# Kernel tuning notes

Measured on AMD Instinct MI355X. Metric: run time of the kernel, lower is better.

## Reference

```python
import jax, jax.numpy as jnp
import numpy as np

STATE_DIM = 1024
INPUT_DIM = 1024
OUTPUT_DIM = 1024
BATCH = 8
SEQ = 2048


def setup_inputs() -> dict:
    key = jax.random.key(0)
    k_x, k_a, k_b, k_w, k_bias = jax.random.split(key, 5)
    x = jax.random.normal(k_x, (BATCH, SEQ, INPUT_DIM), dtype=jnp.float32)
    # diagonal transition a in (0, 0.99) for stability
    A = jax.random.uniform(k_a, (STATE_DIM,), dtype=jnp.float32, minval=0.0, maxval=0.99)
    B = jax.random.normal(k_b, (STATE_DIM, INPUT_DIM), dtype=jnp.float32) / np.sqrt(INPUT_DIM)
    W = jax.random.normal(k_w, (OUTPUT_DIM, STATE_DIM), dtype=jnp.float32) / np.sqrt(STATE_DIM)
    b = jax.random.normal(k_bias, (OUTPUT_DIM,), dtype=jnp.float32) * 0.01
    return {"x": x, "A": A, "B": B, "W": W, "b": b}


def reference(x, A, B, W, b):
    # x: [batch, seq, input_dim]
    # Input projection: u_t = B x_t  -> [batch, seq, state_dim]
    u = jnp.einsum('bld,nd->bln', x, B)
    # Diagonal linear recurrence h_t = A * h_{t-1} + u_t via associative scan.
    # Pair representation (a, b) composes as (a1*a2, a2*b1 + b2).
    aa = jnp.broadcast_to(A, u.shape)

    def combine(c1, c2):
        a1, b1 = c1
        a2, b2 = c2
        return a1 * a2, a2 * b1 + b2

    _, h = jax.lax.associative_scan(combine, (aa, u), axis=1)
    # Output projection: [batch, seq, output_dim]
    return jnp.einsum('bln,on->blo', h, W) + b
```

## Files before the change

kernel.cpp:

```cpp
#include <hip/hip_runtime.h>
#include <stdint.h>

#define BATCH 8
#define SEQ 2048
#define DIM 1024
#define MTOT (BATCH * SEQ)

typedef __attribute__((ext_vector_type(8))) short short8;
typedef __attribute__((ext_vector_type(8))) unsigned short ushort8;
typedef __attribute__((ext_vector_type(4))) float floatx4;


__device__ __forceinline__ unsigned short f2bf(float f) {
  union { float f; unsigned u; } c; c.f = f;
  unsigned u = c.u;
  return (unsigned short)((u + 0x7FFFu + ((u >> 16) & 1u)) >> 16);
}
__device__ __forceinline__ float bf2f(unsigned short h) {
  union { unsigned u; float f; } c; c.u = ((unsigned)h) << 16;
  return c.f;
}

__device__ __forceinline__ void gll16(const void* g, void* l) {
  __builtin_amdgcn_global_load_lds(
      (__attribute__((address_space(1))) void*)(uintptr_t)g,
      (__attribute__((address_space(3))) void*)(uintptr_t)l,
      16, 0, 0);
}


#define X4 (MTOT * DIM / 4)
#define M4 (DIM * DIM / 4)

__global__ __launch_bounds__(256) void cast3_kernel(
    const float* __restrict__ x, const float* __restrict__ B,
    const float* __restrict__ W, unsigned short* __restrict__ xb,
    unsigned short* __restrict__ Bb, unsigned short* __restrict__ Wb) {
  int i = blockIdx.x * 256 + threadIdx.x;
  const float4* s4;
  uint2* d2;
  int li;
  if (i < X4) {
    s4 = (const float4*)x; d2 = (uint2*)xb; li = i;
  } else if (i < X4 + M4) {
    s4 = (const float4*)B; d2 = (uint2*)Bb; li = i - X4;
  } else {
    s4 = (const float4*)W; d2 = (uint2*)Wb; li = i - X4 - M4;
  }
  float4 v = s4[li];
  uint2 o;
  o.x = (unsigned)f2bf(v.x) | ((unsigned)f2bf(v.y) << 16);
  o.y = (unsigned)f2bf(v.z) | ((unsigned)f2bf(v.w) << 16);
  d2[li] = o;
}


__global__ __launch_bounds__(256) void gemm1_fused(
    const unsigned short* __restrict__ A,
    const unsigned short* __restrict__ B,
    unsigned short* __restrict__ u,
    const float* __restrict__ Adiag,
    float* __restrict__ aggbuf) {
  __shared__ unsigned short smem[16384];
  __shared__ float segsum[2][128];
  unsigned short* sA = smem;
  unsigned short* sB = smem + 8192;

  const int tid = threadIdx.x;
  const int wave = tid >> 6, lane = tid & 63;

  const int id = blockIdx.x;
  const int xcd = id & 7, j = id >> 3;
  const int mt = xcd * 16 + (j >> 3);
  const int nt = j & 7;
  const size_t m0 = (size_t)mt * 128;
  const int n0 = nt * 128;

  floatx4 acc[4][4] = {};

  const int srow = wave * 8 + (lane >> 3);
  const int scol = (((lane & 7) ^ ((lane >> 3) & 7)) * 8);
  const unsigned short* gA = A + (m0 + srow) * 1024 + scol;
  const unsigned short* gB = B + ((size_t)n0 + srow) * 1024 + scol;
  unsigned short* lA = sA + wave * 8 * 64;
  unsigned short* lB = sB + wave * 8 * 64;

  const int fr = lane & 15;
  const int frs = fr & 7;
  const int kb = lane >> 4;
  const int wm = (wave & 1) * 64, wn = (wave >> 1) * 64;

  for (int kt = 0; kt < 1024; kt += 64) {
#pragma unroll
    for (int r = 0; r < 4; ++r) {
      gll16(gA + (size_t)r * 32 * 1024 + kt, lA + r * 32 * 64);
      gll16(gB + (size_t)r * 32 * 1024 + kt, lB + r * 32 * 64);
    }
    asm volatile("s_waitcnt vmcnt(0)" ::: "memory");
    __syncthreads();
#pragma unroll
    for (int kk = 0; kk < 64; kk += 32) {
      short8 af[4], bfv[4];
#pragma unroll
      for (int i = 0; i < 4; ++i)
        af[i] = *(const short8*)(sA + (wm + i * 16 + fr) * 64 +
                                 ((((kk >> 3) + kb) ^ frs) * 8));
#pragma unroll
      for (int jj = 0; jj < 4; ++jj)
        bfv[jj] = *(const short8*)(sB + (wn + jj * 16 + fr) * 64 +
                                   ((((kk >> 3) + kb) ^ frs) * 8));
#pragma unroll
      for (int i = 0; i < 4; ++i)
#pragma unroll
        for (int jj = 0; jj < 4; ++jj)
          acc[i][jj] = __builtin_amdgcn_mfma_f32_16x16x32_bf16(
              af[i], bfv[jj], acc[i][jj], 0, 0, 0);
    }
    __syncthreads();
  }

  const int col = lane & 15;
  const int row4 = (lane >> 4) * 4;
  unsigned short* sC = smem;
#pragma unroll
  for (int i = 0; i < 4; ++i)
#pragma unroll
    for (int jj = 0; jj < 4; ++jj)
#pragma unroll
      for (int r = 0; r < 4; ++r)
        sC[(wm + i * 16 + row4 + r) * 128 + wn + jj * 16 + col] =
            f2bf(acc[i][jj][r]);
  __syncthreads();

  const int colv = tid & 127;
  const int seg = tid >> 7;
  const float a = Adiag[n0 + colv];
  {
    float s = 0.f;
    const int t0 = seg * 64;
#pragma unroll 8
    for (int t = 0; t < 64; ++t) {
      int idx = (t0 + t) * 128 + colv;
      s = fmaf(a, s, bf2f(sC[idx]));
      sC[idx] = f2bf(s);
    }
    segsum[seg][colv] = s;
  }
  __syncthreads();

  {
    float a2 = a * a, a4 = a2 * a2, a8 = a4 * a4, a16 = a8 * a8;
    float a32 = a16 * a16, a64 = a32 * a32;
    const float s0 = segsum[0][colv];
    const int t0 = 64 + seg * 32;
    float apow = seg ? a32 * a : a;
#pragma unroll 8
    for (int t = 0; t < 32; ++t) {
      int idx = (t0 + t) * 128 + colv;
      sC[idx] = f2bf(fmaf(apow, s0, bf2f(sC[idx])));
      apow *= a;
    }
    if (seg)
      aggbuf[(size_t)mt * 1024 + n0 + colv] =
          fmaf(a64, s0, segsum[1][colv]);
  }
  __syncthreads();

#pragma unroll
  for (int s = 0; s < 8; ++s) {
    int row = wave * 32 + s * 4 + (lane >> 4);
    int c8 = (lane & 15) * 8;
    *(ushort8*)(u + (m0 + row) * (size_t)1024 + n0 + c8) =
        *(const ushort8*)(sC + row * 128 + c8);
  }
}


__global__ __launch_bounds__(256) void combine_kernel(
    const float* __restrict__ agg, float* __restrict__ carry,
    const float* __restrict__ Adiag) {
  const int id = blockIdx.x * 256 + threadIdx.x;
  const int b = id >> 10, n = id & (DIM - 1);
  float a = Adiag[n];
  float aL = a;
#pragma unroll
  for (int i = 0; i < 7; ++i) aL *= aL;
  float s = 0.f;
#pragma unroll
  for (int c = 0; c < 16; ++c) {
    size_t idx = (size_t)(b * 16 + c) * 1024 + n;
    float local = agg[idx];
    carry[idx] = s;
    s = fmaf(aL, s, local);
  }
}


__global__ __launch_bounds__(256) void apply_kernel(
    unsigned short* __restrict__ u, const float* __restrict__ Adiag,
    const float* __restrict__ carry) {
  const int id = blockIdx.x;
  const int xcd = id & 7, rem = id >> 3;
  const int mt = xcd * 16 + (rem >> 4);
  const int sub = rem & 15;
  const int tg = threadIdx.x >> 7;
  const int ch0 = (threadIdx.x & 127) * 8;

  float a[8], cf[8];
  *(float4*)&a[0] = *(const float4*)(Adiag + ch0);
  *(float4*)&a[4] = *(const float4*)(Adiag + ch0 + 4);
  const float* cp = carry + (size_t)mt * 1024 + ch0;
  *(float4*)&cf[0] = *(const float4*)cp;
  *(float4*)&cf[4] = *(const float4*)(cp + 4);

  const int tl = sub * 8 + tg * 4;
  float apow[8];
#pragma unroll
  for (int j = 0; j < 8; ++j)
    apow[j] = __builtin_amdgcn_exp2f(__builtin_amdgcn_logf(a[j]) *
                                     (float)(tl + 1));
  const size_t base = ((size_t)mt * 128 + tl) * DIM + ch0;
#pragma unroll
  for (int s = 0; s < 4; ++s) {
    ushort8 v = *(const ushort8*)(u + base + (size_t)s * DIM);
    ushort8 o;
#pragma unroll
    for (int j = 0; j < 8; ++j) {
      o[j] = f2bf(fmaf(apow[j], cf[j], bf2f(v[j])));
      apow[j] *= a[j];
    }
    *(ushort8*)(u + base + (size_t)s * DIM) = o;
  }
}


__global__ __launch_bounds__(256) void gemm2(
    const unsigned short* __restrict__ A, const unsigned short* __restrict__ B,
    float* __restrict__ C, const float* __restrict__ bias) {
  __shared__ unsigned short smem[16384];
  unsigned short* sA = smem;
  unsigned short* sB = smem + 8192;

  const int tid = threadIdx.x;
  const int wave = tid >> 6, lane = tid & 63;

  const int id = blockIdx.x;
  const int xcd = id & 7, j = id >> 3;
  const int mt = xcd * 16 + (j >> 3);
  const int nt = j & 7;
  const size_t m0 = (size_t)mt * 128;
  const int n0 = nt * 128;

  floatx4 acc[4][4] = {};

  const int srow = wave * 8 + (lane >> 3);
  const int scol = (((lane & 7) ^ ((lane >> 3) & 7)) * 8);
  const unsigned short* gA = A + (m0 + srow) * 1024 + scol;
  const unsigned short* gB = B + ((size_t)n0 + srow) * 1024 + scol;
  unsigned short* lA = sA + wave * 8 * 64;
  unsigned short* lB = sB + wave * 8 * 64;

  const int fr = lane & 15;
  const int frs = fr & 7;
  const int kb = lane >> 4;
  const int wm = (wave & 1) * 64, wn = (wave >> 1) * 64;

  for (int kt = 0; kt < 1024; kt += 64) {
#pragma unroll
    for (int r = 0; r < 4; ++r) {
      gll16(gA + (size_t)r * 32 * 1024 + kt, lA + r * 32 * 64);
      gll16(gB + (size_t)r * 32 * 1024 + kt, lB + r * 32 * 64);
    }
    asm volatile("s_waitcnt vmcnt(0)" ::: "memory");
    __syncthreads();
#pragma unroll
    for (int kk = 0; kk < 64; kk += 32) {
      short8 af[4], bfv[4];
#pragma unroll
      for (int i = 0; i < 4; ++i)
        af[i] = *(const short8*)(sA + (wm + i * 16 + fr) * 64 +
                                 ((((kk >> 3) + kb) ^ frs) * 8));
#pragma unroll
      for (int jj = 0; jj < 4; ++jj)
        bfv[jj] = *(const short8*)(sB + (wn + jj * 16 + fr) * 64 +
                                   ((((kk >> 3) + kb) ^ frs) * 8));
#pragma unroll
      for (int i = 0; i < 4; ++i)
#pragma unroll
        for (int jj = 0; jj < 4; ++jj)
          acc[i][jj] = __builtin_amdgcn_mfma_f32_16x16x32_bf16(
              af[i], bfv[jj], acc[i][jj], 0, 0, 0);
    }
    __syncthreads();
  }

  const int col = lane & 15;
  const int row4 = (lane >> 4) * 4;
#pragma unroll
  for (int i = 0; i < 4; ++i)
#pragma unroll
    for (int jj = 0; jj < 4; ++jj)
#pragma unroll
      for (int r = 0; r < 4; ++r) {
        size_t m = m0 + wm + i * 16 + row4 + r;
        int n = n0 + wn + jj * 16 + col;
        C[m * 1024 + n] = acc[i][jj][r] + bias[n];
      }
}


extern "C" void kernel_launch(void* const* d_in, const int* in_sizes, int n_in,
                              void* d_out, int out_size, void* d_ws,
                              size_t ws_size, hipStream_t stream) {
  const float* x    = (const float*)d_in[0];
  const float* A    = (const float*)d_in[1];
  const float* B    = (const float*)d_in[2];
  const float* W    = (const float*)d_in[3];
  const float* bias = (const float*)d_in[4];

  char* ws = (char*)d_ws;
  unsigned short* xb   = (unsigned short*)ws;
  unsigned short* ubuf = (unsigned short*)(ws + 33554432);
  unsigned short* Bb   = (unsigned short*)(ws + 67108864);
  unsigned short* Wb   = (unsigned short*)(ws + 69206016);
  float* aggbuf        = (float*)(ws + 71303168);
  float* carry         = (float*)(ws + 71827456);

  cast3_kernel<<<(X4 + 2 * M4) / 256, 256, 0, stream>>>(x, B, W, xb, Bb, Wb);

  gemm1_fused<<<1024, 256, 0, stream>>>(xb, Bb, ubuf, A, aggbuf);

  combine_kernel<<<32, 256, 0, stream>>>(aggbuf, carry, A);

  apply_kernel<<<2048, 256, 0, stream>>>(ubuf, A, carry);

  gemm2<<<1024, 256, 0, stream>>>(ubuf, Wb, (float*)d_out, bias);
}
```

Baseline: 233.4 us.

## Fuse input cast into gemm1 and carry apply into gemm2 tile loads

```diff
diff --git a/kernel.cpp b/kernel.cpp
--- a/kernel.cpp
+++ b/kernel.cpp
@@ -29,23 +29,19 @@
 }
 
 
-#define X4 (MTOT * DIM / 4)
 #define M4 (DIM * DIM / 4)
 
-__global__ __launch_bounds__(256) void cast3_kernel(
-    const float* __restrict__ x, const float* __restrict__ B,
-    const float* __restrict__ W, unsigned short* __restrict__ xb,
+__global__ __launch_bounds__(256) void cast2_kernel(
+    const float* __restrict__ B, const float* __restrict__ W,
     unsigned short* __restrict__ Bb, unsigned short* __restrict__ Wb) {
   int i = blockIdx.x * 256 + threadIdx.x;
   const float4* s4;
   uint2* d2;
   int li;
-  if (i < X4) {
-    s4 = (const float4*)x; d2 = (uint2*)xb; li = i;
-  } else if (i < X4 + M4) {
-    s4 = (const float4*)B; d2 = (uint2*)Bb; li = i - X4;
+  if (i < M4) {
+    s4 = (const float4*)B; d2 = (uint2*)Bb; li = i;
   } else {
-    s4 = (const float4*)W; d2 = (uint2*)Wb; li = i - X4 - M4;
+    s4 = (const float4*)W; d2 = (uint2*)Wb; li = i - M4;
   }
   float4 v = s4[li];
   uint2 o;
@@ -56,7 +52,7 @@
 
 
 __global__ __launch_bounds__(256) void gemm1_fused(
-    const unsigned short* __restrict__ A,
+    const float* __restrict__ X,
     const unsigned short* __restrict__ B,
     unsigned short* __restrict__ u,
     const float* __restrict__ Adiag,
@@ -80,9 +76,9 @@
 
   const int srow = wave * 8 + (lane >> 3);
   const int scol = (((lane & 7) ^ ((lane >> 3) & 7)) * 8);
-  const unsigned short* gA = A + (m0 + srow) * 1024 + scol;
+  const float* gX = X + (m0 + srow) * 1024 + scol;
   const unsigned short* gB = B + ((size_t)n0 + srow) * 1024 + scol;
-  unsigned short* lA = sA + wave * 8 * 64;
+  unsigned short* lA = sA + wave * 8 * 64 + lane * 8;
   unsigned short* lB = sB + wave * 8 * 64;
 
   const int fr = lane & 15;
@@ -91,10 +87,24 @@
   const int wm = (wave & 1) * 64, wn = (wave >> 1) * 64;
 
   for (int kt = 0; kt < 1024; kt += 64) {
+    float4 av[4][2];
 #pragma unroll
     for (int r = 0; r < 4; ++r) {
-      gll16(gA + (size_t)r * 32 * 1024 + kt, lA + r * 32 * 64);
+      const float* p = gX + (size_t)r * 32 * 1024 + kt;
+      av[r][0] = *(const float4*)p;
+      av[r][1] = *(const float4*)(p + 4);
+    }
+#pragma unroll
+    for (int r = 0; r < 4; ++r)
       gll16(gB + (size_t)r * 32 * 1024 + kt, lB + r * 32 * 64);
+#pragma unroll
+    for (int r = 0; r < 4; ++r) {
+      ushort8 o;
+      o[0] = f2bf(av[r][0].x); o[1] = f2bf(av[r][0].y);
+      o[2] = f2bf(av[r][0].z); o[3] = f2bf(av[r][0].w);
+      o[4] = f2bf(av[r][1].x); o[5] = f2bf(av[r][1].y);
+      o[6] = f2bf(av[r][1].z); o[7] = f2bf(av[r][1].w);
+      *(ushort8*)(lA + r * 32 * 64) = o;
     }
     asm volatile("s_waitcnt vmcnt(0)" ::: "memory");
     __syncthreads();
@@ -196,47 +206,11 @@
 }
 
 
-__global__ __launch_bounds__(256) void apply_kernel(
-    unsigned short* __restrict__ u, const float* __restrict__ Adiag,
-    const float* __restrict__ carry) {
-  const int id = blockIdx.x;
-  const int xcd = id & 7, rem = id >> 3;
-  const int mt = xcd * 16 + (rem >> 4);
-  const int sub = rem & 15;
-  const int tg = threadIdx.x >> 7;
-  const int ch0 = (threadIdx.x & 127) * 8;
-
-  float a[8], cf[8];
-  *(float4*)&a[0] = *(const float4*)(Adiag + ch0);
-  *(float4*)&a[4] = *(const float4*)(Adiag + ch0 + 4);
-  const float* cp = carry + (size_t)mt * 1024 + ch0;
-  *(float4*)&cf[0] = *(const float4*)cp;
-  *(float4*)&cf[4] = *(const float4*)(cp + 4);
-
-  const int tl = sub * 8 + tg * 4;
-  float apow[8];
-#pragma unroll
-  for (int j = 0; j < 8; ++j)
-    apow[j] = __builtin_amdgcn_exp2f(__builtin_amdgcn_logf(a[j]) *
-                                     (float)(tl + 1));
-  const size_t base = ((size_t)mt * 128 + tl) * DIM + ch0;
-#pragma unroll
-  for (int s = 0; s < 4; ++s) {
-    ushort8 v = *(const ushort8*)(u + base + (size_t)s * DIM);
-    ushort8 o;
-#pragma unroll
-    for (int j = 0; j < 8; ++j) {
-      o[j] = f2bf(fmaf(apow[j], cf[j], bf2f(v[j])));
-      apow[j] *= a[j];
-    }
-    *(ushort8*)(u + base + (size_t)s * DIM) = o;
-  }
-}
-
-
-__global__ __launch_bounds__(256) void gemm2(
-    const unsigned short* __restrict__ A, const unsigned short* __restrict__ B,
-    float* __restrict__ C, const float* __restrict__ bias) {
+__global__ __launch_bounds__(256) void gemm2_fused(
+    const unsigned short* __restrict__ A,
+    const unsigned short* __restrict__ Bw,
+    float* __restrict__ C, const float* __restrict__ bias,
+    const float* __restrict__ Adiag, const float* __restrict__ carry) {
   __shared__ unsigned short smem[16384];
   unsigned short* sA = smem;
   unsigned short* sB = smem + 8192;
@@ -256,9 +230,10 @@
   const int srow = wave * 8 + (lane >> 3);
   const int scol = (((lane & 7) ^ ((lane >> 3) & 7)) * 8);
   const unsigned short* gA = A + (m0 + srow) * 1024 + scol;
-  const unsigned short* gB = B + ((size_t)n0 + srow) * 1024 + scol;
-  unsigned short* lA = sA + wave * 8 * 64;
+  const unsigned short* gB = Bw + ((size_t)n0 + srow) * 1024 + scol;
+  unsigned short* lA = sA + wave * 8 * 64 + lane * 8;
   unsigned short* lB = sB + wave * 8 * 64;
+  const float* cbase = carry + (size_t)mt * 1024;
 
   const int fr = lane & 15;
   const int frs = fr & 7;
@@ -266,10 +241,36 @@
   const int wm = (wave & 1) * 64, wn = (wave >> 1) * 64;
 
   for (int kt = 0; kt < 1024; kt += 64) {
+    ushort8 hv[4];
+#pragma unroll
+    for (int r = 0; r < 4; ++r)
+      hv[r] = *(const ushort8*)(gA + (size_t)r * 32 * 1024 + kt);
+    float4 la0 = *(const float4*)(Adiag + kt + scol);
+    float4 la1 = *(const float4*)(Adiag + kt + scol + 4);
+    float4 cf0 = *(const float4*)(cbase + kt + scol);
+    float4 cf1 = *(const float4*)(cbase + kt + scol + 4);
+#pragma unroll
+    for (int r = 0; r < 4; ++r)
+      gll16(gB + (size_t)r * 32 * 1024 + kt, lB + r * 32 * 64);
+
+    float la[8] = {la0.x, la0.y, la0.z, la0.w, la1.x, la1.y, la1.z, la1.w};
+    float cf[8] = {cf0.x, cf0.y, cf0.z, cf0.w, cf1.x, cf1.y, cf1.z, cf1.w};
+    float ap[8], a32[8];
+#pragma unroll
+    for (int q = 0; q < 8; ++q) {
+      float lg = __builtin_amdgcn_logf(la[q]);
+      ap[q] = __builtin_amdgcn_exp2f(lg * (float)(srow + 1));
+      a32[q] = __builtin_amdgcn_exp2f(lg * 32.0f);
+    }
 #pragma unroll
     for (int r = 0; r < 4; ++r) {
-      gll16(gA + (size_t)r * 32 * 1024 + kt, lA + r * 32 * 64);
-      gll16(gB + (size_t)r * 32 * 1024 + kt, lB + r * 32 * 64);
+      ushort8 o;
+#pragma unroll
+      for (int q = 0; q < 8; ++q) {
+        o[q] = f2bf(fmaf(ap[q], cf[q], bf2f(hv[r][q])));
+        ap[q] *= a32[q];
+      }
+      *(ushort8*)(lA + r * 32 * 64) = o;
     }
     asm volatile("s_waitcnt vmcnt(0)" ::: "memory");
     __syncthreads();
@@ -319,20 +320,17 @@
   const float* bias = (const float*)d_in[4];
 
   char* ws = (char*)d_ws;
-  unsigned short* xb   = (unsigned short*)ws;
-  unsigned short* ubuf = (unsigned short*)(ws + 33554432);
-  unsigned short* Bb   = (unsigned short*)(ws + 67108864);
-  unsigned short* Wb   = (unsigned short*)(ws + 69206016);
-  float* aggbuf        = (float*)(ws + 71303168);
-  float* carry         = (float*)(ws + 71827456);
-
-  cast3_kernel<<<(X4 + 2 * M4) / 256, 256, 0, stream>>>(x, B, W, xb, Bb, Wb);
-
-  gemm1_fused<<<1024, 256, 0, stream>>>(xb, Bb, ubuf, A, aggbuf);
+  unsigned short* ubuf = (unsigned short*)ws;
+  unsigned short* Bb   = (unsigned short*)(ws + 33554432);
+  unsigned short* Wb   = (unsigned short*)(ws + 35651584);
+  float* aggbuf        = (float*)(ws + 37748736);
+  float* carry         = (float*)(ws + 38273024);
+
+  cast2_kernel<<<2 * M4 / 256, 256, 0, stream>>>(B, W, Bb, Wb);
+
+  gemm1_fused<<<1024, 256, 0, stream>>>(x, Bb, ubuf, A, aggbuf);
 
   combine_kernel<<<32, 256, 0, stream>>>(aggbuf, carry, A);
 
-  apply_kernel<<<2048, 256, 0, stream>>>(ubuf, A, carry);
-
-  gemm2<<<1024, 256, 0, stream>>>(ubuf, Wb, (float*)d_out, bias);
-}
+  gemm2_fused<<<1024, 256, 0, stream>>>(ubuf, Wb, (float*)d_out, bias, A, carry);
+}
```

Measured after the change: 239.2 us. +2.5%, slower.

## Pipeline output GEMM with triple-buffered LDS and larger 256x128 tiles

Applied to the files above, without the earlier changes.

```diff
diff --git a/kernel.cpp b/kernel.cpp
--- a/kernel.cpp
+++ b/kernel.cpp
@@ -234,65 +234,86 @@
 }
 
 
-__global__ __launch_bounds__(256) void gemm2(
-    const unsigned short* __restrict__ A, const unsigned short* __restrict__ B,
+__global__ __launch_bounds__(512, 2) void gemm2_pipe(
+    const unsigned short* __restrict__ A,
+    const unsigned short* __restrict__ Bw,
     float* __restrict__ C, const float* __restrict__ bias) {
-  __shared__ unsigned short smem[16384];
-  unsigned short* sA = smem;
-  unsigned short* sB = smem + 8192;
+  extern __shared__ unsigned short sm[];
 
   const int tid = threadIdx.x;
-  const int wave = tid >> 6, lane = tid & 63;
+  const int wid = tid >> 6, lane = tid & 63;
 
   const int id = blockIdx.x;
   const int xcd = id & 7, j = id >> 3;
-  const int mt = xcd * 16 + (j >> 3);
+  const int mt = xcd * 8 + (j >> 3);
   const int nt = j & 7;
-  const size_t m0 = (size_t)mt * 128;
+  const size_t m0 = (size_t)mt * 256;
   const int n0 = nt * 128;
 
   floatx4 acc[4][4] = {};
 
-  const int srow = wave * 8 + (lane >> 3);
-  const int scol = (((lane & 7) ^ ((lane >> 3) & 7)) * 8);
-  const unsigned short* gA = A + (m0 + srow) * 1024 + scol;
-  const unsigned short* gB = B + ((size_t)n0 + srow) * 1024 + scol;
-  unsigned short* lA = sA + wave * 8 * 64;
-  unsigned short* lB = sB + wave * 8 * 64;
+  const int srow = tid >> 3;
+  const int scolg = (tid & 7) ^ (srow & 7);
+  const unsigned short* gA = A + (m0 + srow) * 1024 + scolg * 8;
+  const unsigned short* gB = Bw + ((size_t)n0 + srow) * 1024 + scolg * 8;
 
   const int fr = lane & 15;
   const int frs = fr & 7;
   const int kb = lane >> 4;
-  const int wm = (wave & 1) * 64, wn = (wave >> 1) * 64;
-
-  for (int kt = 0; kt < 1024; kt += 64) {
-#pragma unroll
-    for (int r = 0; r < 4; ++r) {
-      gll16(gA + (size_t)r * 32 * 1024 + kt, lA + r * 32 * 64);
-      gll16(gB + (size_t)r * 32 * 1024 + kt, lB + r * 32 * 64);
-    }
-    asm volatile("s_waitcnt vmcnt(0)" ::: "memory");
-    __syncthreads();
-#pragma unroll
-    for (int kk = 0; kk < 64; kk += 32) {
-      short8 af[4], bfv[4];
+  const int wm = (wid >> 1) * 64;
+  const int wn = (wid & 1) * 64;
+
+#define G2_STAGE(tt, s)                                                     \
+  {                                                                         \
+    const int kt_ = (tt) * 64;                                              \
+    unsigned short* a_ = sm + (s) * 16384 + wid * 512;                      \
+    unsigned short* b_ = sm + 49152 + (s) * 8192 + wid * 512;               \
+    _Pragma("unroll") for (int r = 0; r < 4; ++r)                           \
+        gll16(gA + (size_t)r * 64 * 1024 + kt_, a_ + r * 4096);             \
+    _Pragma("unroll") for (int r = 0; r < 2; ++r)                           \
+        gll16(gB + (size_t)r * 64 * 1024 + kt_, b_ + r * 4096);             \
+  }
+
+  G2_STAGE(0, 0);
+  G2_STAGE(1, 1);
+  asm volatile("s_waitcnt vmcnt(6)" ::: "memory");
+  __syncthreads();
+
+  for (int t = 0; t < 16; ++t) {
+    if (t + 2 < 16) G2_STAGE(t + 2, (t + 2) % 3);
+
+    const unsigned short* sA = sm + (t % 3) * 16384;
+    const unsigned short* sB = sm + 49152 + (t % 3) * 8192;
+    short8 af[4][2], bfv[4][2];
+#pragma unroll
+    for (int kk = 0; kk < 2; ++kk) {
 #pragma unroll
       for (int i = 0; i < 4; ++i)
-        af[i] = *(const short8*)(sA + (wm + i * 16 + fr) * 64 +
-                                 ((((kk >> 3) + kb) ^ frs) * 8));
+        af[i][kk] = *(const short8*)(sA + (wm + i * 16 + fr) * 64 +
+                                     (((kk * 4 + kb) ^ frs) * 8));
 #pragma unroll
       for (int jj = 0; jj < 4; ++jj)
-        bfv[jj] = *(const short8*)(sB + (wn + jj * 16 + fr) * 64 +
-                                   ((((kk >> 3) + kb) ^ frs) * 8));
+        bfv[jj][kk] = *(const short8*)(sB + (wn + jj * 16 + fr) * 64 +
+                                       (((kk * 4 + kb) ^ frs) * 8));
+    }
+    __builtin_amdgcn_s_setprio(1);
+#pragma unroll
+    for (int kk = 0; kk < 2; ++kk)
 #pragma unroll
       for (int i = 0; i < 4; ++i)
 #pragma unroll
         for (int jj = 0; jj < 4; ++jj)
           acc[i][jj] = __builtin_amdgcn_mfma_f32_16x16x32_bf16(
-              af[i], bfv[jj], acc[i][jj], 0, 0, 0);
-    }
+              af[i][kk], bfv[jj][kk], acc[i][jj], 0, 0, 0);
+    __builtin_amdgcn_s_setprio(0);
+
+    if (t + 2 < 16)
+      asm volatile("s_waitcnt vmcnt(6)" ::: "memory");
+    else
+      asm volatile("s_waitcnt vmcnt(0)" ::: "memory");
     __syncthreads();
   }
+#undef G2_STAGE
 
   const int col = lane & 15;
   const int row4 = (lane >> 4) * 4;
@@ -326,6 +347,13 @@
   float* aggbuf        = (float*)(ws + 71303168);
   float* carry         = (float*)(ws + 71827456);
 
+  static bool attr_set = false;
+  if (!attr_set) {
+    hipFuncSetAttribute(reinterpret_cast<const void*>(gemm2_pipe),
+                        hipFuncAttributeMaxDynamicSharedMemorySize, 147456);
+    attr_set = true;
+  }
+
   cast3_kernel<<<(X4 + 2 * M4) / 256, 256, 0, stream>>>(x, B, W, xb, Bb, Wb);
 
   gemm1_fused<<<1024, 256, 0, stream>>>(xb, Bb, ubuf, A, aggbuf);
@@ -334,5 +362,5 @@
 
   apply_kernel<<<2048, 256, 0, stream>>>(ubuf, A, carry);
 
-  gemm2<<<1024, 256, 0, stream>>>(ubuf, Wb, (float*)d_out, bias);
-}
+  gemm2_pipe<<<512, 512, 147456, stream>>>(ubuf, Wb, (float*)d_out, bias);
+}
```

Result: no change. 229.6 us (-1.7%).
